# Optimization experiments

Hardware: AMD Instinct MI355X
Metric: run time of the kernel (lower is better)

Reference implementation:

```python
import jax, jax.numpy as jnp
import numpy as np

B, N, D = 16, 4096, 128
M = 2048  # codebook size
EPS = 1e-10


def setup_inputs() -> dict:
    key = jax.random.key(0)
    kx, kw = jax.random.split(key)
    x = jax.random.normal(kx, (B, N, D), dtype=jnp.float32)
    # codebook (nn.Embedding weight, kaiming-uniform init ~ uniform(-bound, bound))
    bound = np.sqrt(6.0 / D)
    weight = jax.random.uniform(kw, (M, D), dtype=jnp.float32, minval=-bound, maxval=bound)
    return {"x": x, "weight": weight}


def reference(x, weight):
    b, n, d = x.shape
    m = weight.shape[0]
    q = x.reshape(b * n, d)                       # (bn, d)
    # squared L2 distances: ||q||^2 + ||k||^2 - 2 q.k  (temperature==0 -> argmax of -dist)
    l2_q = jnp.sum(q * q, axis=1, keepdims=True)  # (bn, 1)
    l2_k = jnp.sum(weight * weight, axis=1)       # (m,)
    sim = q @ weight.T                            # (bn, m)  GEMM
    dist = l2_q + l2_k - 2.0 * sim
    indices = jnp.argmin(dist, axis=1)            # (bn,)
    z = weight[indices]                           # onehot @ k == gather
    quantized = z.reshape(b, n, d)
    # straight-through estimator (training path): q + (z - q).detach()
    quantized_st = x + jax.lax.stop_gradient(quantized - x)
    # commitment loss: mse(quantized.detach(), x)
    loss = jnp.mean((jax.lax.stop_gradient(quantized_st) - x) ** 2)
    # perplexity over codebook usage (h == 1 head)
    counts = jnp.zeros((m,), dtype=x.dtype).at[indices].add(1.0)
    p = counts / (b * n)                          # mean of onehot over (b, n)
    perp = jnp.exp(-jnp.sum(p * jnp.log(p + EPS)))[None]  # shape (1,) == 'h'
    out_indices = indices.reshape(b, 1, n)
    return quantized_st, loss, perp, out_indices
```

## Files before the change

### kernel.cpp

```cpp
#include <hip/hip_runtime.h>
#include <hip/hip_bf16.h>
#include <math.h>

#define D_DIM 128
#define M_CODES 2048
#define BN_TOT 65536
#define OUT_LOSS 8388608
#define OUT_PERP 8388609
#define OUT_IDX 8388610
#define MARGIN 2e-3f

#define QB 64

#define WS_L2K 0
#define WS_PHI 8192
#define WS_PLO 532480
#define WS_IDX 1056768
#define WS_PART 1318912
#define WS_CNT 1351680
#define WS_FLAGCNT 1359872
#define WS_FLAGGED 1360896

typedef __bf16 bf16x8 __attribute__((ext_vector_type(8)));
typedef float f32x4 __attribute__((ext_vector_type(4)));

#define GLOAD_LDS16(g, l)                                         \
  __builtin_amdgcn_global_load_lds(                               \
      (const __attribute__((address_space(1))) void*)(g),         \
      (__attribute__((address_space(3))) void*)(l), 16, 0, 0)

__global__ __launch_bounds__(256) void l2_kernel(const float* __restrict__ w,
                                                 float* __restrict__ l2k) {
  int i = blockIdx.x * 256 + threadIdx.x;
  const float4* p = (const float4*)(w + (size_t)i * D_DIM);
  double s = 0.0;
#pragma unroll
  for (int j = 0; j < 32; ++j) {
    float4 v = p[j];
    s += (double)(v.x * v.x);
    s += (double)(v.y * v.y);
    s += (double)(v.z * v.z);
    s += (double)(v.w * v.w);
  }
  l2k[i] = (float)s;
}

__global__ __launch_bounds__(256) void pack_w_frag(const float* __restrict__ w,
                                                   __bf16* __restrict__ phi,
                                                   __bf16* __restrict__ plo) {
  int gid = blockIdx.x * 256 + threadIdx.x;
  int lane = gid & 63;
  int t = gid >> 6;
  int nt = t & 3;
  int ks = (t >> 2) & 3;
  int c64 = t >> 4;
  int code = c64 * 64 + nt * 16 + (lane & 15);
  int koff = ks * 32 + (lane >> 4) * 8;
  const float* src = w + (size_t)code * D_DIM + koff;
  float4 u = *(const float4*)src;
  float4 v = *(const float4*)(src + 4);
  float f[8] = {u.x, u.y, u.z, u.w, v.x, v.y, v.z, v.w};
  bf16x8 h, l;
#pragma unroll
  for (int j = 0; j < 8; ++j) {
    __bf16 hh = (__bf16)f[j];
    h[j] = hh;
    l[j] = (__bf16)(f[j] - (float)hh);
  }
  *(bf16x8*)(phi + (size_t)gid * 8) = h;
  *(bf16x8*)(plo + (size_t)gid * 8) = l;
}

__device__ __forceinline__ void merge_bs(float& b, float& s, int& i,
                                         float ob, float os, int oi) {
  if (ob < b) {
    s = fminf(b, os);
    b = ob;
    i = oi;
  } else if (ob > b) {
    s = fminf(s, ob);
  } else {
    s = b;
    if (oi < i) i = oi;
  }
}

__global__ __launch_bounds__(256, 3) void argmin_mfma(
    const float* __restrict__ x, const __bf16* __restrict__ phi,
    const __bf16* __restrict__ plo, const float* __restrict__ l2k,
    int* __restrict__ best_idx, int* __restrict__ flag_count,
    int* __restrict__ flagged) {
  __shared__ __align__(16) unsigned char ldsB[2][16 * 1024];
  __shared__ float redB[4][32];
  __shared__ float redS[4][32];
  __shared__ int redI[4][32];

  const int tid = threadIdx.x;
  const int wv = tid >> 6;
  const int lane = tid & 63;
  const int col = lane & 15;
  const int quad = lane >> 4;
  const int wc = wv & 1;
  const int wq = wv >> 1;
  const int q0 = blockIdx.x * QB;

  bf16x8 ah[2][4], al[2][4];
#pragma unroll
  for (int mt = 0; mt < 2; ++mt) {
#pragma unroll
    for (int ks = 0; ks < 4; ++ks) {
      const float* xr =
          x + (size_t)(q0 + wq * 32 + 16 * mt + col) * D_DIM + 32 * ks + 8 * quad;
      float4 u = *(const float4*)xr;
      float4 v = *(const float4*)(xr + 4);
      float f[8] = {u.x, u.y, u.z, u.w, v.x, v.y, v.z, v.w};
      bf16x8 h, l;
#pragma unroll
      for (int j = 0; j < 8; ++j) {
        __bf16 hh = (__bf16)f[j];
        h[j] = hh;
        l[j] = (__bf16)(f[j] - (float)hh);
      }
      ah[mt][ks] = h;
      al[mt][ks] = l;
    }
  }

  float m1[2][4], m2[2][4];
  int bi[2][4];
#pragma unroll
  for (int mt = 0; mt < 2; ++mt)
#pragma unroll
    for (int r = 0; r < 4; ++r) {
      m1[mt][r] = 3.4e38f;
      m2[mt][r] = 3.4e38f;
      bi[mt][r] = 0;
    }

  auto stage = [&](int ch, int buf) {
    const int c64 = ch >> 1;
    const int ntb = (ch & 1) * 2;
#pragma unroll
    for (int i = 0; i < 4; ++i) {
      int cid = wv * 4 + i;
      int k2 = cid & 7;
      int gran = c64 * 16 + (k2 >> 1) * 4 + ntb + (k2 & 1);
      const __bf16* src = (cid < 8 ? phi : plo) + (size_t)gran * 512 + lane * 8;
      GLOAD_LDS16(src, &ldsB[buf][cid * 1024]);
    }
  };

  stage(0, 0);
  __syncthreads();

  for (int ch = 0; ch < 64; ++ch) {
    const int buf = ch & 1;
    if (ch < 63) stage(ch + 1, buf ^ 1);

    f32x4 acc[2];
#pragma unroll
    for (int mt = 0; mt < 2; ++mt) acc[mt] = (f32x4){0.f, 0.f, 0.f, 0.f};

#pragma unroll
    for (int ks = 0; ks < 4; ++ks) {
      bf16x8 bh = *(const bf16x8*)&ldsB[buf][(ks * 2 + wc) * 1024 + lane * 16];
      bf16x8 bl = *(const bf16x8*)&ldsB[buf][(8 + ks * 2 + wc) * 1024 + lane * 16];
#pragma unroll
      for (int mt = 0; mt < 2; ++mt) {
        acc[mt] = __builtin_amdgcn_mfma_f32_16x16x32_bf16(al[mt][ks], bh, acc[mt], 0, 0, 0);
        acc[mt] = __builtin_amdgcn_mfma_f32_16x16x32_bf16(ah[mt][ks], bl, acc[mt], 0, 0, 0);
        acc[mt] = __builtin_amdgcn_mfma_f32_16x16x32_bf16(ah[mt][ks], bh, acc[mt], 0, 0, 0);
      }
    }

    const int ci = ch * 32 + wc * 16 + col;
    const float l2 = l2k[ci];
#pragma unroll
    for (int mt = 0; mt < 2; ++mt) {
#pragma unroll
      for (int r = 0; r < 4; ++r) {
        float dd = fmaf(-2.0f, acc[mt][r], l2);
        bool lt = dd < m1[mt][r];
        m2[mt][r] = lt ? m1[mt][r] : fminf(m2[mt][r], dd);
        bi[mt][r] = lt ? ci : bi[mt][r];
        m1[mt][r] = fminf(m1[mt][r], dd);
      }
    }

    __syncthreads();
  }

#pragma unroll
  for (int mt = 0; mt < 2; ++mt) {
#pragma unroll
    for (int r = 0; r < 4; ++r) {
      float b = m1[mt][r], s = m2[mt][r];
      int i = bi[mt][r];
#pragma unroll
      for (int m = 1; m < 16; m <<= 1) {
        float ob = __shfl_xor(b, m);
        float os = __shfl_xor(s, m);
        int oi = __shfl_xor(i, m);
        merge_bs(b, s, i, ob, os, oi);
      }
      if (col == 0) {
        int qloc = 16 * mt + 4 * quad + r;
        redB[wv][qloc] = b;
        redS[wv][qloc] = s;
        redI[wv][qloc] = i;
      }
    }
  }
  __syncthreads();

  if (tid < QB) {
    int wq2 = tid >> 5;
    int ql = tid & 31;
    float b = 3.4e38f, s = 3.4e38f;
    int i = 0x7fffffff;
    merge_bs(b, s, i, redB[wq2 * 2 + 0][ql], redS[wq2 * 2 + 0][ql], redI[wq2 * 2 + 0][ql]);
    merge_bs(b, s, i, redB[wq2 * 2 + 1][ql], redS[wq2 * 2 + 1][ql], redI[wq2 * 2 + 1][ql]);
    best_idx[q0 + tid] = i;
    if (s - b < MARGIN) {
      int pos = atomicAdd(flag_count, 1);
      flagged[pos] = q0 + tid;
    }
  }
}

__global__ __launch_bounds__(256) void fixup_kernel(const float* __restrict__ x,
                                                    const float* __restrict__ w,
                                                    const float* __restrict__ l2k32,
                                                    const int* __restrict__ flagged,
                                                    const int* __restrict__ flag_count,
                                                    int* __restrict__ best_idx) {
  __shared__ float qs[D_DIM];
  __shared__ float l2q_sh;
  __shared__ float redD[256];
  __shared__ int redI[256];
  const int tid = threadIdx.x;
  const int n = *flag_count;
  for (int f = blockIdx.x; f < n; f += gridDim.x) {
    __syncthreads();
    int q = flagged[f];
    if (tid < D_DIM) qs[tid] = x[(size_t)q * D_DIM + tid];
    __syncthreads();
    if (tid == 0) {
      double s = 0.0;
      for (int d = 0; d < D_DIM; ++d) {
        float t = qs[d] * qs[d];
        s += (double)t;
      }
      l2q_sh = (float)s;
    }
    __syncthreads();
    const float l2q = l2q_sh;
    float bd = 3.4e38f;
    int bi = 0x7fffffff;
    for (int c = tid; c < M_CODES; c += 256) {
      const float4* wr = (const float4*)(w + (size_t)c * D_DIM);
      double s = 0.0;
#pragma unroll
      for (int j = 0; j < 32; ++j) {
        float4 v = wr[j];
        s = fma((double)qs[j * 4 + 0], (double)v.x, s);
        s = fma((double)qs[j * 4 + 1], (double)v.y, s);
        s = fma((double)qs[j * 4 + 2], (double)v.z, s);
        s = fma((double)qs[j * 4 + 3], (double)v.w, s);
      }
      float simf = (float)s;
      float S = l2q + l2k32[c];
      float T = 2.0f * simf;
      float dist = S - T;
      if (dist < bd) { bd = dist; bi = c; }
    }
    redD[tid] = bd;
    redI[tid] = bi;
    __syncthreads();
    for (int off = 128; off; off >>= 1) {
      if (tid < off) {
        float od = redD[tid + off];
        int oi = redI[tid + off];
        if (od < redD[tid] || (od == redD[tid] && oi < redI[tid])) {
          redD[tid] = od;
          redI[tid] = oi;
        }
      }
      __syncthreads();
    }
    if (tid == 0) best_idx[q] = redI[0];
  }
}

__global__ __launch_bounds__(256) void epilogue_kernel(const float* __restrict__ x,
                                                       const float* __restrict__ w,
                                                       const int* __restrict__ best_idx,
                                                       float* __restrict__ out,
                                                       float* __restrict__ part,
                                                       int* __restrict__ counts) {
  int gid = blockIdx.x * 256 + threadIdx.x;
  int q = gid >> 5;
  int d4 = gid & 31;
  int idx = best_idx[q];
  float4 xv = ((const float4*)x)[gid];
  float4 wv = ((const float4*)w)[(size_t)idx * 32 + d4];
  float4 o;
  float t0 = wv.x - xv.x; o.x = xv.x + t0; float e0 = o.x - xv.x;
  float t1 = wv.y - xv.y; o.y = xv.y + t1; float e1 = o.y - xv.y;
  float t2 = wv.z - xv.z; o.z = xv.z + t2; float e2 = o.z - xv.z;
  float t3 = wv.w - xv.w; o.w = xv.w + t3; float e3 = o.w - xv.w;
  float ls = e0 * e0 + e1 * e1 + e2 * e2 + e3 * e3;
  ((float4*)out)[gid] = o;

  for (int off = 32; off; off >>= 1) ls += __shfl_down(ls, off);
  __shared__ float red[4];
  if ((threadIdx.x & 63) == 0) red[threadIdx.x >> 6] = ls;
  __syncthreads();
  if (threadIdx.x == 0) part[blockIdx.x] = red[0] + red[1] + red[2] + red[3];

  if (d4 == 0) {
    out[OUT_IDX + q] = (float)idx;
    atomicAdd(&counts[idx], 1);
  }
}

__global__ __launch_bounds__(256) void finalize_kernel(const int* __restrict__ counts,
                                                       const float* __restrict__ part,
                                                       float* __restrict__ out) {
  int tid = threadIdx.x;
  float ls = 0.f;
  for (int i = tid; i < 8192; i += 256) ls += part[i];
  float es = 0.f;
  for (int i = tid; i < M_CODES; i += 256) {
    float p = (float)counts[i] * (1.0f / 65536.0f);
    es += p * logf(p + 1e-10f);
  }
  for (int off = 32; off; off >>= 1) {
    ls += __shfl_down(ls, off);
    es += __shfl_down(es, off);
  }
  __shared__ float redl[4], rede[4];
  if ((tid & 63) == 0) {
    redl[tid >> 6] = ls;
    rede[tid >> 6] = es;
  }
  __syncthreads();
  if (tid == 0) {
    out[OUT_LOSS] = (redl[0] + redl[1] + redl[2] + redl[3]) * (1.0f / 8388608.0f);
    out[OUT_PERP] = expf(-(rede[0] + rede[1] + rede[2] + rede[3]));
  }
}

extern "C" void kernel_launch(void* const* d_in, const int* in_sizes, int n_in,
                              void* d_out, int out_size, void* d_ws, size_t ws_size,
                              hipStream_t stream) {
  const float* x = (const float*)d_in[0];
  const float* w = (const float*)d_in[1];
  float* out = (float*)d_out;
  char* ws = (char*)d_ws;
  float* l2k = (float*)(ws + WS_L2K);
  __bf16* phi = (__bf16*)(ws + WS_PHI);
  __bf16* plo = (__bf16*)(ws + WS_PLO);
  int* bidx = (int*)(ws + WS_IDX);
  float* part = (float*)(ws + WS_PART);
  int* counts = (int*)(ws + WS_CNT);
  int* flagcnt = (int*)(ws + WS_FLAGCNT);
  int* flagged = (int*)(ws + WS_FLAGGED);

  hipMemsetAsync(counts, 0, M_CODES * sizeof(int), stream);
  hipMemsetAsync(flagcnt, 0, sizeof(int), stream);
  l2_kernel<<<8, 256, 0, stream>>>(w, l2k);
  pack_w_frag<<<128, 256, 0, stream>>>(w, phi, plo);
  argmin_mfma<<<BN_TOT / QB, 256, 0, stream>>>(x, phi, plo, l2k, bidx, flagcnt, flagged);
  fixup_kernel<<<256, 256, 0, stream>>>(x, w, l2k, flagged, flagcnt, bidx);
  epilogue_kernel<<<8192, 256, 0, stream>>>(x, w, bidx, out, part, counts);
  finalize_kernel<<<1, 256, 0, stream>>>(counts, part, out);
}
```

Before: 251.9 us.

## Pack codebook per-chunk contiguously and fold l2k into MFMA accumulator init

The codebook hi/lo bf16 fragments are now packed into one buffer laid out chunk by chunk, so each wave stages four contiguous 1KB pieces with simple address math. The distance is reformulated as maximizing q·k − ½‖k‖², with the accumulator seeded by −½l2k, which removes the per-element fma. Only the winning chunk index is tracked per lane. The loop is manually unrolled by two with fixed buffers, l2k loads are prefetched one iteration ahead, and occupancy is raised to 4 blocks per CU. The flag margin is rescaled to match the halved distance, and the higher occupancy target may add register pressure.

```diff
diff --git a/kernel.cpp b/kernel.cpp
--- a/kernel.cpp
+++ b/kernel.cpp
@@ -13,8 +13,7 @@
 #define QB 64
 
 #define WS_L2K 0
-#define WS_PHI 8192
-#define WS_PLO 532480
+#define WS_PB 8192
 #define WS_IDX 1056768
 #define WS_PART 1318912
 #define WS_CNT 1351680
@@ -28,6 +27,8 @@
   __builtin_amdgcn_global_load_lds(                               \
       (const __attribute__((address_space(1))) void*)(g),         \
       (__attribute__((address_space(3))) void*)(l), 16, 0, 0)
+
+#define MFMA16(a, b, c) __builtin_amdgcn_mfma_f32_16x16x32_bf16((a), (b), (c), 0, 0, 0)
 
 __global__ __launch_bounds__(256) void l2_kernel(const float* __restrict__ w,
                                                  float* __restrict__ l2k) {
@@ -45,52 +46,50 @@
   l2k[i] = (float)s;
 }
 
-__global__ __launch_bounds__(256) void pack_w_frag(const float* __restrict__ w,
-                                                   __bf16* __restrict__ phi,
-                                                   __bf16* __restrict__ plo) {
+__global__ __launch_bounds__(256) void pack_w_chunk(const float* __restrict__ w,
+                                                    __bf16* __restrict__ pb) {
   int gid = blockIdx.x * 256 + threadIdx.x;
   int lane = gid & 63;
-  int t = gid >> 6;
-  int nt = t & 3;
-  int ks = (t >> 2) & 3;
-  int c64 = t >> 4;
-  int code = c64 * 64 + nt * 16 + (lane & 15);
+  int g = gid >> 6;
+  int cid = g & 15;
+  int ch = g >> 4;
+  int k2 = cid & 7;
+  int ks = k2 >> 1;
+  int wc = k2 & 1;
+  int code = ch * 32 + wc * 16 + (lane & 15);
   int koff = ks * 32 + (lane >> 4) * 8;
   const float* src = w + (size_t)code * D_DIM + koff;
   float4 u = *(const float4*)src;
   float4 v = *(const float4*)(src + 4);
   float f[8] = {u.x, u.y, u.z, u.w, v.x, v.y, v.z, v.w};
-  bf16x8 h, l;
+  bf16x8 o;
 #pragma unroll
   for (int j = 0; j < 8; ++j) {
     __bf16 hh = (__bf16)f[j];
-    h[j] = hh;
-    l[j] = (__bf16)(f[j] - (float)hh);
-  }
-  *(bf16x8*)(phi + (size_t)gid * 8) = h;
-  *(bf16x8*)(plo + (size_t)gid * 8) = l;
+    o[j] = (cid < 8) ? hh : (__bf16)(f[j] - (float)hh);
+  }
+  *(bf16x8*)(pb + (size_t)g * 512 + lane * 8) = o;
 }
 
 __device__ __forceinline__ void merge_bs(float& b, float& s, int& i,
                                          float ob, float os, int oi) {
-  if (ob < b) {
-    s = fminf(b, os);
+  if (ob > b) {
+    s = fmaxf(b, os);
     b = ob;
     i = oi;
-  } else if (ob > b) {
-    s = fminf(s, ob);
+  } else if (ob < b) {
+    s = fmaxf(s, ob);
   } else {
     s = b;
     if (oi < i) i = oi;
   }
 }
 
-__global__ __launch_bounds__(256, 3) void argmin_mfma(
-    const float* __restrict__ x, const __bf16* __restrict__ phi,
-    const __bf16* __restrict__ plo, const float* __restrict__ l2k,
-    int* __restrict__ best_idx, int* __restrict__ flag_count,
-    int* __restrict__ flagged) {
-  __shared__ __align__(16) unsigned char ldsB[2][16 * 1024];
+__global__ __launch_bounds__(256, 4) void argmin_mfma(
+    const float* __restrict__ x, const __bf16* __restrict__ pb,
+    const float* __restrict__ l2k, int* __restrict__ best_idx,
+    int* __restrict__ flag_count, int* __restrict__ flagged) {
+  __shared__ __align__(16) unsigned char ldsB[2][16384];
   __shared__ float redB[4][32];
   __shared__ float redS[4][32];
   __shared__ int redI[4][32];
@@ -127,66 +126,77 @@
   }
 
   float m1[2][4], m2[2][4];
-  int bi[2][4];
+  int bc[2][4];
 #pragma unroll
   for (int mt = 0; mt < 2; ++mt)
 #pragma unroll
     for (int r = 0; r < 4; ++r) {
-      m1[mt][r] = 3.4e38f;
-      m2[mt][r] = 3.4e38f;
-      bi[mt][r] = 0;
-    }
+      m1[mt][r] = -3.4e38f;
+      m2[mt][r] = -3.4e38f;
+      bc[mt][r] = 0;
+    }
+
+  const char* pbase = (const char*)pb + (size_t)(wv * 4) * 1024 + (size_t)lane * 16;
+  const int ldsw = wc * 1024 + lane * 16;
+  const float* l2p = l2k + wc * 16 + col;
 
   auto stage = [&](int ch, int buf) {
-    const int c64 = ch >> 1;
-    const int ntb = (ch & 1) * 2;
-#pragma unroll
-    for (int i = 0; i < 4; ++i) {
-      int cid = wv * 4 + i;
-      int k2 = cid & 7;
-      int gran = c64 * 16 + (k2 >> 1) * 4 + ntb + (k2 & 1);
-      const __bf16* src = (cid < 8 ? phi : plo) + (size_t)gran * 512 + lane * 8;
-      GLOAD_LDS16(src, &ldsB[buf][cid * 1024]);
-    }
+    const char* s = pbase + (size_t)ch * 16384;
+    unsigned char* d = &ldsB[buf][(wv * 4) * 1024];
+    GLOAD_LDS16(s, d);
+    GLOAD_LDS16(s + 1024, d + 1024);
+    GLOAD_LDS16(s + 2048, d + 2048);
+    GLOAD_LDS16(s + 3072, d + 3072);
   };
 
+  auto compute = [&](int ch, int buf, float l2v) {
+    float ini = -0.5f * l2v;
+    f32x4 acc[2];
+    acc[0] = (f32x4){ini, ini, ini, ini};
+    acc[1] = (f32x4){ini, ini, ini, ini};
+#pragma unroll
+    for (int ks = 0; ks < 4; ++ks) {
+      const unsigned char* base = &ldsB[buf][ks * 2048 + ldsw];
+      bf16x8 bh = *(const bf16x8*)(base);
+      bf16x8 bl = *(const bf16x8*)(base + 8192);
+#pragma unroll
+      for (int mt = 0; mt < 2; ++mt) {
+        acc[mt] = MFMA16(al[mt][ks], bh, acc[mt]);
+        acc[mt] = MFMA16(ah[mt][ks], bl, acc[mt]);
+        acc[mt] = MFMA16(ah[mt][ks], bh, acc[mt]);
+      }
+    }
+#pragma unroll
+    for (int mt = 0; mt < 2; ++mt) {
+#pragma unroll
+      for (int r = 0; r < 4; ++r) {
+        float dd = acc[mt][r];
+        bool gt = dd > m1[mt][r];
+        m2[mt][r] = fmaxf(m2[mt][r], fminf(m1[mt][r], dd));
+        bc[mt][r] = gt ? ch : bc[mt][r];
+        m1[mt][r] = fmaxf(m1[mt][r], dd);
+      }
+    }
+  };
+
   stage(0, 0);
+  float l2n0 = l2p[0];
+  float l2n1 = l2p[32];
   __syncthreads();
 
-  for (int ch = 0; ch < 64; ++ch) {
-    const int buf = ch & 1;
-    if (ch < 63) stage(ch + 1, buf ^ 1);
-
-    f32x4 acc[2];
-#pragma unroll
-    for (int mt = 0; mt < 2; ++mt) acc[mt] = (f32x4){0.f, 0.f, 0.f, 0.f};
-
-#pragma unroll
-    for (int ks = 0; ks < 4; ++ks) {
-      bf16x8 bh = *(const bf16x8*)&ldsB[buf][(ks * 2 + wc) * 1024 + lane * 16];
-      bf16x8 bl = *(const bf16x8*)&ldsB[buf][(8 + ks * 2 + wc) * 1024 + lane * 16];
-#pragma unroll
-      for (int mt = 0; mt < 2; ++mt) {
-        acc[mt] = __builtin_amdgcn_mfma_f32_16x16x32_bf16(al[mt][ks], bh, acc[mt], 0, 0, 0);
-        acc[mt] = __builtin_amdgcn_mfma_f32_16x16x32_bf16(ah[mt][ks], bl, acc[mt], 0, 0, 0);
-        acc[mt] = __builtin_amdgcn_mfma_f32_16x16x32_bf16(ah[mt][ks], bh, acc[mt], 0, 0, 0);
-      }
-    }
-
-    const int ci = ch * 32 + wc * 16 + col;
-    const float l2 = l2k[ci];
-#pragma unroll
-    for (int mt = 0; mt < 2; ++mt) {
-#pragma unroll
-      for (int r = 0; r < 4; ++r) {
-        float dd = fmaf(-2.0f, acc[mt][r], l2);
-        bool lt = dd < m1[mt][r];
-        m2[mt][r] = lt ? m1[mt][r] : fminf(m2[mt][r], dd);
-        bi[mt][r] = lt ? ci : bi[mt][r];
-        m1[mt][r] = fminf(m1[mt][r], dd);
-      }
-    }
-
+#pragma unroll 1
+  for (int cc = 0; cc < 32; ++cc) {
+    const int ch0 = cc * 2;
+    float l2c0 = l2n0, l2c1 = l2n1;
+    if (cc < 31) {
+      l2n0 = l2p[(ch0 + 2) * 32];
+      l2n1 = l2p[(ch0 + 3) * 32];
+    }
+    stage(ch0 + 1, 1);
+    compute(ch0, 0, l2c0);
+    __syncthreads();
+    if (cc < 31) stage(ch0 + 2, 0);
+    compute(ch0 + 1, 1, l2c1);
     __syncthreads();
   }
 
@@ -195,7 +205,7 @@
 #pragma unroll
     for (int r = 0; r < 4; ++r) {
       float b = m1[mt][r], s = m2[mt][r];
-      int i = bi[mt][r];
+      int i = bc[mt][r] * 32 + wc * 16 + col;
 #pragma unroll
       for (int m = 1; m < 16; m <<= 1) {
         float ob = __shfl_xor(b, m);
@@ -216,12 +226,12 @@
   if (tid < QB) {
     int wq2 = tid >> 5;
     int ql = tid & 31;
-    float b = 3.4e38f, s = 3.4e38f;
+    float b = -3.4e38f, s = -3.4e38f;
     int i = 0x7fffffff;
     merge_bs(b, s, i, redB[wq2 * 2 + 0][ql], redS[wq2 * 2 + 0][ql], redI[wq2 * 2 + 0][ql]);
     merge_bs(b, s, i, redB[wq2 * 2 + 1][ql], redS[wq2 * 2 + 1][ql], redI[wq2 * 2 + 1][ql]);
     best_idx[q0 + tid] = i;
-    if (s - b < MARGIN) {
+    if (2.0f * (b - s) < MARGIN) {
       int pos = atomicAdd(flag_count, 1);
       flagged[pos] = q0 + tid;
     }
@@ -359,8 +369,7 @@
   float* out = (float*)d_out;
   char* ws = (char*)d_ws;
   float* l2k = (float*)(ws + WS_L2K);
-  __bf16* phi = (__bf16*)(ws + WS_PHI);
-  __bf16* plo = (__bf16*)(ws + WS_PLO);
+  __bf16* pb = (__bf16*)(ws + WS_PB);
   int* bidx = (int*)(ws + WS_IDX);
   float* part = (float*)(ws + WS_PART);
   int* counts = (int*)(ws + WS_CNT);
@@ -370,8 +379,8 @@
   hipMemsetAsync(counts, 0, M_CODES * sizeof(int), stream);
   hipMemsetAsync(flagcnt, 0, sizeof(int), stream);
   l2_kernel<<<8, 256, 0, stream>>>(w, l2k);
-  pack_w_frag<<<128, 256, 0, stream>>>(w, phi, plo);
-  argmin_mfma<<<BN_TOT / QB, 256, 0, stream>>>(x, phi, plo, l2k, bidx, flagcnt, flagged);
+  pack_w_chunk<<<256, 256, 0, stream>>>(w, pb);
+  argmin_mfma<<<BN_TOT / QB, 256, 0, stream>>>(x, pb, l2k, bidx, flagcnt, flagged);
   fixup_kernel<<<256, 256, 0, stream>>>(x, w, l2k, flagged, flagcnt, bidx);
   epilogue_kernel<<<8192, 256, 0, stream>>>(x, w, bidx, out, part, counts);
   finalize_kernel<<<1, 256, 0, stream>>>(counts, part, out);
```

New measurement: 259.5 us. 1.03x slower.
